# Performance work log

Measured on AMD Instinct MI355X. Metric: run time of the kernel, lower is better.

## Reference

```python
import jax, jax.numpy as jnp
import numpy as np

H = 256

def setup_inputs() -> dict:
    key = jax.random.key(0)
    ks = jax.random.split(key, 8)
    B, S = 32, 4096
    hidden = jax.random.normal(ks[0], (B, H), dtype=jnp.float32)
    encoder_outputs = jax.random.normal(ks[1], (B, S, H), dtype=jnp.float32)
    scale = 1.0 / np.sqrt(H)
    W1_w = jax.random.uniform(ks[2], (H, H), jnp.float32, -scale, scale)
    W1_b = jax.random.uniform(ks[3], (H,), jnp.float32, -scale, scale)
    W2_w = jax.random.uniform(ks[4], (H, H), jnp.float32, -scale, scale)
    W2_b = jax.random.uniform(ks[5], (H,), jnp.float32, -scale, scale)
    V_w = jax.random.uniform(ks[6], (H, 1), jnp.float32, -scale, scale)
    V_b = jax.random.uniform(ks[7], (1,), jnp.float32, -scale, scale)
    return {"hidden": hidden, "encoder_outputs": encoder_outputs,
            "W1_w": W1_w, "W1_b": W1_b, "W2_w": W2_w, "W2_b": W2_b,
            "V_w": V_w, "V_b": V_b}

def reference(hidden, encoder_outputs, W1_w, W1_b, W2_w, W2_b, V_w, V_b):
    # hidden: (B,H), encoder_outputs: (B,S,H)
    q = hidden @ W1_w + W1_b                     # (B,H)
    k = jnp.einsum('bsh,hd->bsd', encoder_outputs, W2_w) + W2_b  # (B,S,H)
    energy = jnp.tanh(q[:, None, :] + k)         # (B,S,H)
    scores = jnp.einsum('bsh,ho->bso', energy, V_w) + V_b        # (B,S,1)
    attention_weights = jax.nn.softmax(scores, axis=1)           # (B,S,1)
    context_vector = jnp.einsum('bso,bsh->bh', attention_weights, encoder_outputs)  # (B,H)
    return attention_weights, context_vector
```

## Files before the change

kernel.cpp:

```cpp
#include <hip/hip_runtime.h>
#include <hip/hip_bf16.h>
#include <math.h>

#define BB 32
#define SS 4096
#define HH 256

typedef __bf16 bf16x8 __attribute__((ext_vector_type(8)));
typedef float f32x4 __attribute__((ext_vector_type(4)));

#define GLOBAL_AS __attribute__((address_space(1)))
#define LDS_AS    __attribute__((address_space(3)))

__device__ inline bf16x8 cvt8(const float4& x, const float4& y) {
    union { __hip_bfloat162 p[4]; bf16x8 v; } u;
    u.p[0] = __float22bfloat162_rn(make_float2(x.x, x.y));
    u.p[1] = __float22bfloat162_rn(make_float2(x.z, x.w));
    u.p[2] = __float22bfloat162_rn(make_float2(y.x, y.y));
    u.p[3] = __float22bfloat162_rn(make_float2(y.z, y.w));
    return u.v;
}

__device__ inline float fast_tanh(float x) {
    float xc = fminf(fmaxf(x, -10.f), 10.f);
    float e  = __expf(2.f * xc);
    return (e - 1.f) * __builtin_amdgcn_rcpf(e + 1.f);
}

__global__ void prep_kernel(const float* __restrict__ W2_w,
                            ushort* __restrict__ w2sw,
                            const float* __restrict__ hidden,
                            const float* __restrict__ W1_w,
                            const float* __restrict__ W1_b,
                            const float* __restrict__ W2_b,
                            const float* __restrict__ V_w,
                            float* __restrict__ qq,
                            float* __restrict__ Mout) {
    __shared__ float red[HH];
    const int t = threadIdx.x;
    if (blockIdx.x < 256) {
        const int i = blockIdx.x * 256 + t;
        const int j    = i & 7;
        const int lane = (i >> 3) & 63;
        const int nt   = (i >> 9) & 15;
        const int kc   = i >> 13;
        const int k = kc * 32 + ((lane >> 4) & 3) * 8 + j;
        const int n = nt * 16 + (lane & 15);
        __hip_bfloat16 h = __float2bfloat16(W2_w[k * HH + n]);
        w2sw[i] = *(ushort*)&h;
    } else if (blockIdx.x < 256 + BB) {
        const int b = blockIdx.x - 256;
        red[t] = hidden[b * HH + t];
        __syncthreads();
        float acc = 0.f;
#pragma unroll 16
        for (int k = 0; k < HH; ++k)
            acc = fmaf(red[k], W1_w[k * HH + t], acc);
        qq[b * HH + t] = acc + W1_b[t] + W2_b[t];
    } else {
        red[t] = fabsf(V_w[t]);
        __syncthreads();
        for (int off = 128; off > 0; off >>= 1) {
            if (t < off) red[t] += red[t + off];
            __syncthreads();
        }
        if (t == 0) Mout[0] = red[0];
    }
}

__global__ __launch_bounds__(256, 4)
void score_ctx_kernel(const float* __restrict__ enc,
                      const ushort* __restrict__ w2sw,
                      const float* __restrict__ qq,
                      const float* __restrict__ V_w,
                      const float* __restrict__ Mptr,
                      float* __restrict__ wtilde,
                      float* __restrict__ part) {
    __shared__ ushort w2buf[2][8192];
    __shared__ float sc_lds[64];
    __shared__ float accl[4][HH];

    const int t    = threadIdx.x;
    const int b    = blockIdx.y;
    const int c    = blockIdx.x;
    const int s0   = c * 64;
    const int wave = t >> 6;
    const int lane = t & 63;
    const int mw   = wave & 1;
    const int nw   = wave >> 1;
    const int l15  = lane & 15;
    const int quad = lane >> 4;

    f32x4 acc[2][8];
#pragma unroll
    for (int mt = 0; mt < 2; ++mt)
#pragma unroll
        for (int nt = 0; nt < 8; ++nt) acc[mt][nt] = (f32x4)0.f;

    {
        const char* gsrc = (const char*)w2sw + t * 16;
        char* ldst = (char*)&w2buf[0][0] + wave * 1024;
#pragma unroll
        for (int i = 0; i < 4; ++i)
            __builtin_amdgcn_global_load_lds(
                (const GLOBAL_AS void*)(gsrc + i * 4096),
                (LDS_AS void*)(ldst + i * 4096), 16, 0, 0);
    }

    const float* aptr0 =
        enc + ((size_t)(b * SS + s0 + mw * 32 + l15)) * HH + quad * 8;
    const float* aptr1 = aptr0 + (size_t)16 * HH;
    float4 ax0 = *(const float4*)aptr0, ay0 = *(const float4*)(aptr0 + 4);
    float4 ax1 = *(const float4*)aptr1, ay1 = *(const float4*)(aptr1 + 4);

    for (int kc = 0; kc < 8; ++kc) {
        const int cur = kc & 1;
        __syncthreads();
        if (kc < 7) {
            const char* gsrc = (const char*)w2sw + (kc + 1) * 16384 + t * 16;
            char* ldst = (char*)&w2buf[cur ^ 1][0] + wave * 1024;
#pragma unroll
            for (int i = 0; i < 4; ++i)
                __builtin_amdgcn_global_load_lds(
                    (const GLOBAL_AS void*)(gsrc + i * 4096),
                    (LDS_AS void*)(ldst + i * 4096), 16, 0, 0);
        }
        bf16x8 af0 = cvt8(ax0, ay0);
        bf16x8 af1 = cvt8(ax1, ay1);
        if (kc < 7) {
            const int o = (kc + 1) * 32;
            ax0 = *(const float4*)(aptr0 + o);
            ay0 = *(const float4*)(aptr0 + o + 4);
            ax1 = *(const float4*)(aptr1 + o);
            ay1 = *(const float4*)(aptr1 + o + 4);
        }
#pragma unroll
        for (int nt = 0; nt < 8; ++nt) {
            bf16x8 bf =
                *(const bf16x8*)&w2buf[cur][((nw * 8 + nt) * 64 + lane) * 8];
            acc[0][nt] = __builtin_amdgcn_mfma_f32_16x16x32_bf16(af0, bf, acc[0][nt], 0, 0, 0);
            acc[1][nt] = __builtin_amdgcn_mfma_f32_16x16x32_bf16(af1, bf, acc[1][nt], 0, 0, 0);
        }
    }

    float p[2][4] = {{0.f, 0.f, 0.f, 0.f}, {0.f, 0.f, 0.f, 0.f}};
#pragma unroll
    for (int nt = 0; nt < 8; ++nt) {
        const int n = nw * 128 + nt * 16 + l15;
        const float qn = qq[b * HH + n];
        const float vn = V_w[n];
#pragma unroll
        for (int mt = 0; mt < 2; ++mt)
#pragma unroll
            for (int r = 0; r < 4; ++r)
                p[mt][r] = fmaf(vn, fast_tanh(qn + acc[mt][nt][r]), p[mt][r]);
    }
#pragma unroll
    for (int off = 1; off < 16; off <<= 1)
#pragma unroll
        for (int mt = 0; mt < 2; ++mt)
#pragma unroll
            for (int r = 0; r < 4; ++r)
                p[mt][r] += __shfl_xor(p[mt][r], off);

    if (nw == 0 && l15 == 0) {
#pragma unroll
        for (int mt = 0; mt < 2; ++mt)
            *(float4*)&sc_lds[mw * 32 + mt * 16 + quad * 4] =
                make_float4(p[mt][0], p[mt][1], p[mt][2], p[mt][3]);
    }
    __syncthreads();
    const float Mv = Mptr[0];
    if (nw == 1 && l15 == 0) {
#pragma unroll
        for (int mt = 0; mt < 2; ++mt) {
            const int row = mw * 32 + mt * 16 + quad * 4;
            float4 h = *(const float4*)&sc_lds[row];
            float4 v = make_float4(__expf(h.x + p[mt][0] - Mv),
                                   __expf(h.y + p[mt][1] - Mv),
                                   __expf(h.z + p[mt][2] - Mv),
                                   __expf(h.w + p[mt][3] - Mv));
            *(float4*)&sc_lds[row] = v;
            *(float4*)&wtilde[b * SS + s0 + row] = v;
        }
    }
    __syncthreads();

    const int tr = t >> 6;
    const int h0 = (t & 63) * 4;
    float4 a = make_float4(0.f, 0.f, 0.f, 0.f);
    const float* ep = enc + ((size_t)(b * SS + s0)) * HH;
#pragma unroll
    for (int jj = 0; jj < 16; ++jj) {
        const int j = jj * 4 + tr;
        const float4 e = *(const float4*)(ep + (size_t)j * HH + h0);
        const float w = sc_lds[j];
        a.x = fmaf(w, e.x, a.x);
        a.y = fmaf(w, e.y, a.y);
        a.z = fmaf(w, e.z, a.z);
        a.w = fmaf(w, e.w, a.w);
    }
    *(float4*)&accl[tr][h0] = a;
    __syncthreads();

    part[((size_t)(b * 64 + c)) * HH + t] =
        accl[0][t] + accl[1][t] + accl[2][t] + accl[3][t];
}

__global__ __launch_bounds__(256)
void finish_kernel(const float* __restrict__ wtilde,
                   const float* __restrict__ part,
                   float* __restrict__ weights_out,
                   float* __restrict__ ctx_out) {
    __shared__ float red[256];
    __shared__ float linv_s;
    const int b = blockIdx.x;
    const int t = threadIdx.x;

    const float4* wt4 = (const float4*)(wtilde + (size_t)b * SS);
    float4 vals[4];
    float l = 0.f;
#pragma unroll
    for (int i = 0; i < 4; ++i) {
        vals[i] = wt4[i * 256 + t];
        l += vals[i].x + vals[i].y + vals[i].z + vals[i].w;
    }
    red[t] = l;
    __syncthreads();
    for (int off = 128; off > 0; off >>= 1) {
        if (t < off) red[t] += red[t + off];
        __syncthreads();
    }
    if (t == 0) linv_s = 1.f / red[0];
    __syncthreads();
    const float linv = linv_s;

    float4* wo4 = (float4*)(weights_out + (size_t)b * SS);
#pragma unroll
    for (int i = 0; i < 4; ++i) {
        const float4 v = vals[i];
        wo4[i * 256 + t] =
            make_float4(v.x * linv, v.y * linv, v.z * linv, v.w * linv);
    }

    float a = 0.f;
#pragma unroll 8
    for (int c = 0; c < 64; ++c)
        a += part[((size_t)(b * 64 + c)) * HH + t];
    ctx_out[b * HH + t] = a * linv;
}

extern "C" void kernel_launch(void* const* d_in, const int* in_sizes, int n_in,
                              void* d_out, int out_size, void* d_ws, size_t ws_size,
                              hipStream_t stream) {
    const float* hidden = (const float*)d_in[0];
    const float* enc    = (const float*)d_in[1];
    const float* W1_w   = (const float*)d_in[2];
    const float* W1_b   = (const float*)d_in[3];
    const float* W2_w   = (const float*)d_in[4];
    const float* W2_b   = (const float*)d_in[5];
    const float* V_w    = (const float*)d_in[6];
    const float* V_b    = (const float*)d_in[7];
    (void)V_b;

    float* out_weights = (float*)d_out;
    float* out_ctx     = (float*)d_out + BB * SS;

    float* ws      = (float*)d_ws;
    float* ws_qq   = ws;
    float* ws_wt   = ws_qq + BB * HH;
    float* ws_part = ws_wt + BB * SS;
    float* ws_M    = ws_part + BB * 64 * HH;
    ushort* ws_w2  = (ushort*)(ws_M + 4);

    prep_kernel<<<dim3(256 + BB + 1), dim3(256), 0, stream>>>(
        W2_w, ws_w2, hidden, W1_w, W1_b, W2_b, V_w, ws_qq, ws_M);
    score_ctx_kernel<<<dim3(SS / 64, BB), dim3(256), 0, stream>>>(
        enc, ws_w2, ws_qq, V_w, ws_M, ws_wt, ws_part);
    finish_kernel<<<dim3(BB), dim3(256), 0, stream>>>(
        ws_wt, ws_part, out_weights, out_ctx);
}
```

Baseline: 247.2 us.

## Load W2 fragments directly into registers instead of staging through LDS

The score kernel stops staging W2 tiles into LDS with global_load_lds and block barriers. Each wave now loads its bf16 W2 fragments straight from global memory into double-buffered registers alongside the encoder prefetch, so the per-chunk __syncthreads goes away. The launch bound is relaxed from 4 to 2 blocks per SM to make room for the extra registers, and unnormalised weights are written directly into the output buffer instead of a workspace. The cost is higher register pressure and lower occupancy, plus redundant global/L2 reads of W2 across waves.

```diff
diff --git a/kernel.cpp b/kernel.cpp
--- a/kernel.cpp
+++ b/kernel.cpp
@@ -8,9 +8,6 @@
 
 typedef __bf16 bf16x8 __attribute__((ext_vector_type(8)));
 typedef float f32x4 __attribute__((ext_vector_type(4)));
-
-#define GLOBAL_AS __attribute__((address_space(1)))
-#define LDS_AS    __attribute__((address_space(3)))
 
 __device__ inline bf16x8 cvt8(const float4& x, const float4& y) {
     union { __hip_bfloat162 p[4]; bf16x8 v; } u;
@@ -68,15 +65,14 @@
     }
 }
 
-__global__ __launch_bounds__(256, 4)
+__global__ __launch_bounds__(256, 2)
 void score_ctx_kernel(const float* __restrict__ enc,
                       const ushort* __restrict__ w2sw,
                       const float* __restrict__ qq,
                       const float* __restrict__ V_w,
                       const float* __restrict__ Mptr,
-                      float* __restrict__ wtilde,
+                      float* __restrict__ wtilde_out,
                       float* __restrict__ part) {
-    __shared__ ushort w2buf[2][8192];
     __shared__ float sc_lds[64];
     __shared__ float accl[4][HH];
 
@@ -97,49 +93,42 @@
 #pragma unroll
         for (int nt = 0; nt < 8; ++nt) acc[mt][nt] = (f32x4)0.f;
 
-    {
-        const char* gsrc = (const char*)w2sw + t * 16;
-        char* ldst = (char*)&w2buf[0][0] + wave * 1024;
-#pragma unroll
-        for (int i = 0; i < 4; ++i)
-            __builtin_amdgcn_global_load_lds(
-                (const GLOBAL_AS void*)(gsrc + i * 4096),
-                (LDS_AS void*)(ldst + i * 4096), 16, 0, 0);
-    }
-
+    const bf16x8* bgl = (const bf16x8*)w2sw + (size_t)(nw * 8) * 64 + lane;
     const float* aptr0 =
         enc + ((size_t)(b * SS + s0 + mw * 32 + l15)) * HH + quad * 8;
     const float* aptr1 = aptr0 + (size_t)16 * HH;
-    float4 ax0 = *(const float4*)aptr0, ay0 = *(const float4*)(aptr0 + 4);
-    float4 ax1 = *(const float4*)aptr1, ay1 = *(const float4*)(aptr1 + 4);
-
+
+    bf16x8 bq[2][8];
+    float4 ax[2][2], ay[2][2];
+
+#pragma unroll
+    for (int nt = 0; nt < 8; ++nt) bq[0][nt] = bgl[nt * 64];
+    ax[0][0] = *(const float4*)aptr0;
+    ay[0][0] = *(const float4*)(aptr0 + 4);
+    ax[0][1] = *(const float4*)aptr1;
+    ay[0][1] = *(const float4*)(aptr1 + 4);
+
+#pragma unroll
     for (int kc = 0; kc < 8; ++kc) {
         const int cur = kc & 1;
-        __syncthreads();
         if (kc < 7) {
-            const char* gsrc = (const char*)w2sw + (kc + 1) * 16384 + t * 16;
-            char* ldst = (char*)&w2buf[cur ^ 1][0] + wave * 1024;
-#pragma unroll
-            for (int i = 0; i < 4; ++i)
-                __builtin_amdgcn_global_load_lds(
-                    (const GLOBAL_AS void*)(gsrc + i * 4096),
-                    (LDS_AS void*)(ldst + i * 4096), 16, 0, 0);
-        }
-        bf16x8 af0 = cvt8(ax0, ay0);
-        bf16x8 af1 = cvt8(ax1, ay1);
-        if (kc < 7) {
+#pragma unroll
+            for (int nt = 0; nt < 8; ++nt)
+                bq[cur ^ 1][nt] = bgl[(kc + 1) * 1024 + nt * 64];
             const int o = (kc + 1) * 32;
-            ax0 = *(const float4*)(aptr0 + o);
-            ay0 = *(const float4*)(aptr0 + o + 4);
-            ax1 = *(const float4*)(aptr1 + o);
-            ay1 = *(const float4*)(aptr1 + o + 4);
-        }
+            ax[cur ^ 1][0] = *(const float4*)(aptr0 + o);
+            ay[cur ^ 1][0] = *(const float4*)(aptr0 + o + 4);
+            ax[cur ^ 1][1] = *(const float4*)(aptr1 + o);
+            ay[cur ^ 1][1] = *(const float4*)(aptr1 + o + 4);
+        }
+        bf16x8 af0 = cvt8(ax[cur][0], ay[cur][0]);
+        bf16x8 af1 = cvt8(ax[cur][1], ay[cur][1]);
 #pragma unroll
         for (int nt = 0; nt < 8; ++nt) {
-            bf16x8 bf =
-                *(const bf16x8*)&w2buf[cur][((nw * 8 + nt) * 64 + lane) * 8];
-            acc[0][nt] = __builtin_amdgcn_mfma_f32_16x16x32_bf16(af0, bf, acc[0][nt], 0, 0, 0);
-            acc[1][nt] = __builtin_amdgcn_mfma_f32_16x16x32_bf16(af1, bf, acc[1][nt], 0, 0, 0);
+            acc[0][nt] = __builtin_amdgcn_mfma_f32_16x16x32_bf16(
+                af0, bq[cur][nt], acc[0][nt], 0, 0, 0);
+            acc[1][nt] = __builtin_amdgcn_mfma_f32_16x16x32_bf16(
+                af1, bq[cur][nt], acc[1][nt], 0, 0, 0);
         }
     }
 
@@ -181,7 +170,7 @@
                                    __expf(h.z + p[mt][2] - Mv),
                                    __expf(h.w + p[mt][3] - Mv));
             *(float4*)&sc_lds[row] = v;
-            *(float4*)&wtilde[b * SS + s0 + row] = v;
+            *(float4*)&wtilde_out[b * SS + s0 + row] = v;
         }
     }
     __syncthreads();
@@ -208,8 +197,7 @@
 }
 
 __global__ __launch_bounds__(256)
-void finish_kernel(const float* __restrict__ wtilde,
-                   const float* __restrict__ part,
+void finish_kernel(const float* __restrict__ part,
                    float* __restrict__ weights_out,
                    float* __restrict__ ctx_out) {
     __shared__ float red[256];
@@ -217,12 +205,12 @@
     const int b = blockIdx.x;
     const int t = threadIdx.x;
 
-    const float4* wt4 = (const float4*)(wtilde + (size_t)b * SS);
+    float4* wo4 = (float4*)(weights_out + (size_t)b * SS);
     float4 vals[4];
     float l = 0.f;
 #pragma unroll
     for (int i = 0; i < 4; ++i) {
-        vals[i] = wt4[i * 256 + t];
+        vals[i] = wo4[i * 256 + t];
         l += vals[i].x + vals[i].y + vals[i].z + vals[i].w;
     }
     red[t] = l;
@@ -235,7 +223,6 @@
     __syncthreads();
     const float linv = linv_s;
 
-    float4* wo4 = (float4*)(weights_out + (size_t)b * SS);
 #pragma unroll
     for (int i = 0; i < 4; ++i) {
         const float4 v = vals[i];
@@ -268,15 +255,14 @@
 
     float* ws      = (float*)d_ws;
     float* ws_qq   = ws;
-    float* ws_wt   = ws_qq + BB * HH;
-    float* ws_part = ws_wt + BB * SS;
+    float* ws_part = ws_qq + BB * HH;
     float* ws_M    = ws_part + BB * 64 * HH;
     ushort* ws_w2  = (ushort*)(ws_M + 4);
 
     prep_kernel<<<dim3(256 + BB + 1), dim3(256), 0, stream>>>(
         W2_w, ws_w2, hidden, W1_w, W1_b, W2_b, V_w, ws_qq, ws_M);
     score_ctx_kernel<<<dim3(SS / 64, BB), dim3(256), 0, stream>>>(
-        enc, ws_w2, ws_qq, V_w, ws_M, ws_wt, ws_part);
+        enc, ws_w2, ws_qq, V_w, ws_M, out_weights, ws_part);
     finish_kernel<<<dim3(BB), dim3(256), 0, stream>>>(
-        ws_wt, ws_part, out_weights, out_ctx);
-}
+        ws_part, out_weights, out_ctx);
+}
```

New measurement: 253.3 us. 2.5% more time.
